# Kernel optimization log

Hardware: AMD Instinct MI355X
Metric: run time of the kernel (lower is better)

## Reference

```python
import jax, jax.numpy as jnp
import numpy as np
from jax.scipy.special import gammaln, logsumexp

T, K, D = 262144, 32, 64


def setup_inputs() -> dict:
    key = jax.random.key(0)
    ks = jax.random.split(key, 7)
    Y = jax.random.normal(ks[0], (T, D), dtype=jnp.float32)
    dT = jax.random.uniform(ks[1], (T,), dtype=jnp.float32) + 0.01  # strictly positive intervals
    A = jax.random.normal(ks[2], (K, K), dtype=jnp.float32)
    log_ab = jax.random.normal(ks[3], (K, 2), dtype=jnp.float32) * 0.5
    mu = jax.random.normal(ks[4], (K, D), dtype=jnp.float32)
    log_sigma = jax.random.normal(ks[5], (K, D), dtype=jnp.float32) * 0.1
    pi = jax.random.normal(ks[6], (K,), dtype=jnp.float32)
    return {"Y": Y, "dT": dT, "A": A, "log_ab": log_ab, "mu": mu, "log_sigma": log_sigma, "pi": pi}


def _gamma_ll(dT, log_ab):
    # per-state Gamma(concentration=exp(log_ab[:,0]), rate=exp(log_ab[:,1])) log_prob -> [T, K]
    a = jnp.exp(log_ab[:, 0])
    b = jnp.exp(log_ab[:, 1])
    const = a * log_ab[:, 1] - gammaln(a)  # a*log(b) - lgamma(a)
    return const[None, :] + jnp.log(dT)[:, None] * (a - 1.0)[None, :] - dT[:, None] * b[None, :]


def _gauss_ll(Y, mu, log_sigma):
    # diagonal-Gaussian emission log-likelihood summed over D, via GEMMs -> [T, K]
    inv_var = jnp.exp(-2.0 * log_sigma)  # [K, D]
    quad = (-0.5) * (Y * Y) @ inv_var.T + Y @ (mu * inv_var).T - 0.5 * jnp.sum(mu * mu * inv_var, axis=-1)[None, :]
    const = -jnp.sum(log_sigma, axis=-1) - 0.5 * D * jnp.log(2.0 * jnp.pi).astype(Y.dtype)
    return quad + const[None, :]


def _hmm_lognorm(pi0, logA, ll):
    # log-domain forward algorithm; returns log normalizer (scalar)
    alpha0 = pi0 + ll[0]

    def step(alpha, ll_t):
        # alpha_t[j] = logsumexp_i(alpha[i] + logA[i, j]) + ll_t[j]
        alpha = logsumexp(alpha[:, None] + logA, axis=0) + ll_t
        return alpha, None

    alphaT, _ = jax.lax.scan(step, alpha0, ll[1:])
    return logsumexp(alphaT)


def reference(Y, dT, A, log_ab, mu, log_sigma, pi):
    h = Y  # obs_model embedding (identity for Gaussian emission model)
    y_ll = _gauss_ll(Y, mu, log_sigma)          # [T, K]
    y_loss = jnp.zeros((), dtype=Y.dtype)
    dT_ll = _gamma_ll(dT, log_ab)               # [T, K]
    ll = y_ll + dT_ll
    logA = jax.nn.log_softmax(A, axis=1)        # LogSoftmax(dim=1)(A)
    pi0 = jax.nn.log_softmax(pi, axis=0)        # LogSoftmax(dim=0)(pi)
    loss = -1.0 * _hmm_lognorm(pi0, logA, ll) + y_loss
    return h, loss
```

## Files before the change

### kernel.cpp

```cpp
#include <hip/hip_runtime.h>
#include <stdint.h>

#define TT 262144
#define KK 32
#define DD 64
#define LSTEP 32
#define PCH 8192
#define YSTRIDE 68

typedef __attribute__((ext_vector_type(4)))  float f4v;
typedef __attribute__((ext_vector_type(16))) float f16v;
typedef __attribute__((ext_vector_type(4)))  short s4v;
typedef __attribute__((ext_vector_type(2)))  int   i2v;
typedef __attribute__((ext_vector_type(2)))  unsigned int u2v;
typedef __attribute__((ext_vector_type(4)))  unsigned int u4v;

#define WS_AFRAG_US 0
#define WS_WFRAG_US 1024
#define WS_WF    2560
#define WS_CK    6656
#define WS_AM1   6688
#define WS_BB    6720
#define WS_PI0   6752
#define WS_LS    8192
#define WS_LS2   16384
#define SH_MATS  33280
#define SH_MATS2 (33280 + PCH*1024)
#define LN2F 0.69314718055994531f

__device__ __forceinline__ unsigned pkbf(float hi, float lo) {
    return __builtin_amdgcn_perm(__builtin_bit_cast(unsigned, hi),
                                 __builtin_bit_cast(unsigned, lo), 0x07060302u);
}
__device__ __forceinline__ unsigned short f2bf_rne(float f) {
    unsigned u = __builtin_bit_cast(unsigned, f);
    unsigned r = u + 0x7FFFu + ((u >> 16) & 1u);
    return (unsigned short)(r >> 16);
}
__device__ __forceinline__ float bf2f(unsigned short u) {
    return __builtin_bit_cast(float, (unsigned)u << 16);
}
__device__ __forceinline__ float wmax32(float v) {
    v = fmaxf(v, __shfl_xor(v, 1));  v = fmaxf(v, __shfl_xor(v, 2));
    v = fmaxf(v, __shfl_xor(v, 4));  v = fmaxf(v, __shfl_xor(v, 8));
    v = fmaxf(v, __shfl_xor(v, 16));
    return v;
}
__device__ __forceinline__ float wmax64(float v) {
    v = wmax32(v); v = fmaxf(v, __shfl_xor(v, 32));
    return v;
}
__device__ __forceinline__ float wsum32(float v) {
    v += __shfl_xor(v, 1); v += __shfl_xor(v, 2); v += __shfl_xor(v, 4);
    v += __shfl_xor(v, 8); v += __shfl_xor(v, 16);
    return v;
}
__device__ __forceinline__ float wsum64(float v) {
    v = wsum32(v); v += __shfl_xor(v, 32);
    return v;
}
__device__ __forceinline__ float wval(int dd, int k, const float* mu, const float* lsg) {
    int d = dd & 63;
    float lv = lsg[k * DD + d];
    float iv = __expf(-2.f * lv);
    return (dd < DD) ? (-0.5f * iv) : (mu[k * DD + d] * iv);
}

__global__ void k0_prep(const float* __restrict__ Y, const float* __restrict__ A,
                        const float* __restrict__ lab, const float* __restrict__ mu,
                        const float* __restrict__ lsg, const float* __restrict__ pi,
                        float* __restrict__ ws, float* __restrict__ out)
{
    __shared__ float lseA[KK];
    const int tid = threadIdx.x;
    if (tid < KK) {
        float m = -1e30f;
        for (int j = 0; j < KK; ++j) m = fmaxf(m, A[tid * KK + j]);
        float s = 0.f;
        for (int j = 0; j < KK; ++j) s += __expf(A[tid * KK + j] - m);
        lseA[tid] = m + __logf(s);

        float mp = -1e30f;
        for (int j = 0; j < KK; ++j) mp = fmaxf(mp, pi[j]);
        float sp = 0.f;
        for (int j = 0; j < KK; ++j) sp += __expf(pi[j] - mp);
        ws[WS_PI0 + tid] = pi[tid] - (mp + __logf(sp));

        float la = lab[tid * 2 + 0], lb = lab[tid * 2 + 1];
        float a = __expf(la), b = __expf(lb);
        float c1 = 0.f, c2 = 0.f;
        for (int d = 0; d < DD; ++d) {
            float lv = lsg[tid * DD + d];
            float mv = mu[tid * DD + d];
            c1 -= lv;
            c2 += mv * mv * __expf(-2.f * lv);
        }
        ws[WS_CK + tid]  = a * lb - lgammaf(a) + c1 - 0.5f * c2 - 32.f * 1.8378770664093453f;
        ws[WS_AM1 + tid] = a - 1.f;
        ws[WS_BB + tid]  = b;
    }
    __syncthreads();
    unsigned short* us = (unsigned short*)ws;
    for (int idx = tid; idx < 1024; idx += 256) {
        int g = idx >> 8, rem = idx & 255, ln = rem >> 2, e = rem & 3;
        int m = 8 * g + 4 * (ln >> 5) + e, i = ln & 31;
        us[WS_AFRAG_US + idx] = f2bf_rne(__expf(A[m * KK + i] - lseA[m]));
    }
    for (int idx = tid; idx < 4096; idx += 256) {
        int s = idx >> 8, rem = idx & 255, ln = rem >> 2, e = rem & 3;
        int dd = 8 * s + 4 * (ln >> 5) + e, k = ln & 31;
        us[WS_WFRAG_US + idx] = f2bf_rne(wval(dd, k, mu, lsg));
    }
    for (int idx = tid; idx < 4096; idx += 256) {
        int dd = idx >> 5, k = idx & 31;
        ws[WS_WF + idx] = wval(dd, k, mu, lsg);
    }
    if (tid < DD) out[tid] = Y[tid];
}

__global__ __launch_bounds__(256, 4) void k1_scan(
    const float* __restrict__ Y, const float* __restrict__ dTp,
    float* __restrict__ ws, float* __restrict__ out)
{
    __shared__ __align__(16) float Yt[4][32 * YSTRIDE];
    __shared__ __align__(16) float dtv[4][32], dtl[4][32];

    const int tid = threadIdx.x;
    const int wv = tid >> 6, l = tid & 63, h = l >> 5, c = l & 31;
    const int p = blockIdx.x * 4 + wv;
    const int t0 = 1 + p * LSTEP;
    const int nsteps = min(LSTEP, TT - t0);

    const unsigned short* afr = (const unsigned short*)ws + WS_AFRAG_US;
    const unsigned short* wfr = (const unsigned short*)ws + WS_WFRAG_US;

    const float cK = ws[WS_CK + c], am1 = ws[WS_AM1 + c], bb = ws[WS_BB + c];

    if (l < 32) {
        int t = t0 + l;
        float dv = (t < TT) ? dTp[t] : 1.f;
        dtv[wv][l] = dv;
        dtl[wv][l] = __logf(dv);
    }

    f16v zf;
    #pragma unroll
    for (int r = 0; r < 16; ++r) zf[r] = 0.f;

    {
        const size_t gbase = (size_t)t0 * DD;
        const int r = (l >> 4);
        const int col = (l & 15) * 4;
        #pragma unroll
        for (int i = 0; i < 8; ++i) {
            const size_t gi = gbase + (size_t)i * 256 + l * 4;
            f4v y4; y4[0] = 0.f; y4[1] = 0.f; y4[2] = 0.f; y4[3] = 0.f;
            const bool ok = gi < (size_t)TT * DD;
            if (ok) y4 = *(const f4v*)(Y + gi);
            if (ok) *(f4v*)(out + gi) = y4;
            *(f4v*)(&Yt[wv][(i * 4 + r) * YSTRIDE + col]) = y4;
        }
    }

    f16v acc = zf;
    s4v rawf[8];
    #pragma unroll
    for (int g = 0; g < 8; ++g) {
        const f4v y4 = *(const f4v*)(&Yt[wv][c * YSTRIDE + 8 * g + 4 * h]);
        const f4v q4 = y4 * y4;
        i2v sq; sq[0] = pkbf(q4[1], q4[0]); sq[1] = pkbf(q4[3], q4[2]);
        i2v rw; rw[0] = pkbf(y4[1], y4[0]); rw[1] = pkbf(y4[3], y4[2]);
        rawf[g] = __builtin_bit_cast(s4v, rw);
        s4v wf = *(const s4v*)(wfr + g * 256 + l * 4);
        acc = __builtin_amdgcn_mfma_f32_32x32x8bf16_1k(__builtin_bit_cast(s4v, sq), wf, acc, 0, 0, 0);
    }
    #pragma unroll
    for (int g = 0; g < 8; ++g) {
        s4v wf = *(const s4v*)(wfr + (8 + g) * 256 + l * 4);
        acc = __builtin_amdgcn_mfma_f32_32x32x8bf16_1k(rawf[g], wf, acc, 0, 0, 0);
    }

    s4v aF[4];
    #pragma unroll
    for (int g = 0; g < 4; ++g) aF[g] = *(const s4v*)(afr + g * 256 + l * 4);

    float csv = 0.f;
    #pragma unroll
    for (int m = 0; m < 4; ++m) {
        const f4v dv4 = *(const f4v*)(&dtv[wv][8 * m + 4 * h]);
        const f4v dl4 = *(const f4v*)(&dtl[wv][8 * m + 4 * h]);
        #pragma unroll
        for (int j = 0; j < 4; ++j) {
            const int row = 8 * m + 4 * h + j;
            float llv = acc[4 * m + j] + cK + am1 * dl4[j] - bb * dv4[j];
            float cm = wmax32(llv);
            Yt[wv][row * YSTRIDE + c] = __expf(llv - cm);
            csv += (row < nsteps) ? cm : 0.f;
        }
    }
    float cacc = wsum64(csv) * (1.f / 32.f);

    asm volatile("s_waitcnt lgkmcnt(0)" ::: "memory");

    f16v S;
    #pragma unroll
    for (int m = 0; m < 4; ++m)
        #pragma unroll
        for (int j = 0; j < 4; ++j)
            S[4 * m + j] = ((8 * m + 4 * h + j) == c) ? 1.f : 0.f;
    float l2acc = 0.f;

    auto step = [&](int n) {
        f16v Dv = zf;
        #pragma unroll
        for (int g = 0; g < 4; ++g) {
            i2v bd; bd[0] = pkbf(S[4 * g + 1], S[4 * g + 0]);
                    bd[1] = pkbf(S[4 * g + 3], S[4 * g + 2]);
            Dv = __builtin_amdgcn_mfma_f32_32x32x8bf16_1k(aF[g], __builtin_bit_cast(s4v, bd), Dv, 0, 0, 0);
        }
        #pragma unroll
        for (int m = 0; m < 4; ++m) {
            const f4v e4 = *(const f4v*)(&Yt[wv][n * YSTRIDE + 8 * m + 4 * h]);
            #pragma unroll
            for (int j = 0; j < 4; ++j) S[4 * m + j] = Dv[4 * m + j] * e4[j];
        }
    };
    auto rescale = [&]() {
        float mx = S[0];
        #pragma unroll
        for (int r = 1; r < 16; ++r) mx = fmaxf(mx, S[r]);
        mx = wmax64(mx);
        const float inv = __fdividef(1.f, mx);
        #pragma unroll
        for (int r = 0; r < 16; ++r) S[r] *= inv;
        l2acc += __log2f(mx);
    };

    if (p != PCH - 1) {
        #pragma unroll
        for (int n = 0; n < LSTEP; ++n) {
            step(n);
            if ((n & 3) == 3) rescale();
        }
    } else {
        for (int n = 0; n < nsteps; ++n) {
            step(n);
            if ((n & 3) == 3) rescale();
        }
    }

    unsigned short* Tb = (unsigned short*)&Yt[wv][0];
    asm volatile("s_waitcnt lgkmcnt(0)" ::: "memory");
    #pragma unroll
    for (int m = 0; m < 4; ++m)
        #pragma unroll
        for (int j = 0; j < 4; ++j)
            Tb[(8 * m + 4 * h + j) * 36 + c] = f2bf_rne(S[4 * m + j]);
    asm volatile("s_waitcnt lgkmcnt(0)" ::: "memory");
    u2v tg[4];
    #pragma unroll
    for (int g = 0; g < 4; ++g)
        tg[g] = *(const u2v*)(Tb + c * 36 + 8 * g + 4 * h);
    unsigned short* gm = (unsigned short*)ws + SH_MATS + (size_t)p * 1024 + l * 16;
    u4v s0; s0[0] = tg[0][0]; s0[1] = tg[0][1]; s0[2] = tg[1][0]; s0[3] = tg[1][1];
    u4v s1; s1[0] = tg[2][0]; s1[1] = tg[2][1]; s1[2] = tg[3][0]; s1[3] = tg[3][1];
    *(u4v*)(gm) = s0;
    *(u4v*)(gm + 8) = s1;
    if (l == 0) ws[WS_LS + p] = cacc + LN2F * l2acc;
}

__device__ __forceinline__ f16v prodAU(const u4v a0, const u4v a1, const f16v U, const f16v zf) {
    s4v aA[4];
    u2v t;
    t[0] = a0[0]; t[1] = a0[1]; aA[0] = __builtin_bit_cast(s4v, t);
    t[0] = a0[2]; t[1] = a0[3]; aA[1] = __builtin_bit_cast(s4v, t);
    t[0] = a1[0]; t[1] = a1[1]; aA[2] = __builtin_bit_cast(s4v, t);
    t[0] = a1[2]; t[1] = a1[3]; aA[3] = __builtin_bit_cast(s4v, t);
    f16v Dv = zf;
    #pragma unroll
    for (int g = 0; g < 4; ++g) {
        i2v bd; bd[0] = pkbf(U[4 * g + 1], U[4 * g + 0]);
                bd[1] = pkbf(U[4 * g + 3], U[4 * g + 2]);
        Dv = __builtin_amdgcn_mfma_f32_32x32x8bf16_1k(aA[g], __builtin_bit_cast(s4v, bd), Dv, 0, 0, 0);
    }
    return Dv;
}

__global__ __launch_bounds__(128, 1) void k2_combine(float* __restrict__ ws)
{
    __shared__ __align__(16) unsigned short slot[2][1152];
    __shared__ float scl[2], lac[2];
    const int tid = threadIdx.x, wv = tid >> 6, l = tid & 63, h = l >> 5, c = l & 31;
    const int blk = blockIdx.x;
    const int idx0 = blk * 64 + wv * 32;
    const unsigned short* mats = (const unsigned short*)ws + SH_MATS;

    float lsv = (l < 32) ? ws[WS_LS + idx0 + l] : 0.f;
    float lssum = wsum64(lsv);

    f16v zf;
    #pragma unroll
    for (int r = 0; r < 16; ++r) zf[r] = 0.f;
    f16v U;
    #pragma unroll
    for (int m = 0; m < 4; ++m)
        #pragma unroll
        for (int j = 0; j < 4; ++j)
            U[4 * m + j] = ((8 * m + 4 * h + j) == c) ? 1.f : 0.f;
    float l2a = 0.f;

    u4v pf[2][2];
    {
        const u4v* mp0 = (const u4v*)(mats + (size_t)idx0 * 1024) + l * 2;
        const u4v* mp1 = (const u4v*)(mats + (size_t)(idx0 + 1) * 1024) + l * 2;
        pf[0][0] = mp0[0]; pf[0][1] = mp0[1];
        pf[1][0] = mp1[0]; pf[1][1] = mp1[1];
    }
    for (int q = 0; q < 32; ++q) {
        const u4v a0 = pf[q & 1][0], a1 = pf[q & 1][1];
        if (q + 2 < 32) {
            const u4v* mp = (const u4v*)(mats + (size_t)(idx0 + q + 2) * 1024) + l * 2;
            pf[q & 1][0] = mp[0]; pf[q & 1][1] = mp[1];
        }
        f16v Dv = prodAU(a0, a1, U, zf);
        if ((q & 3) == 3) {
            float mx = Dv[0];
            #pragma unroll
            for (int r = 1; r < 16; ++r) mx = fmaxf(mx, Dv[r]);
            mx = wmax64(mx);
            const float inv = __fdividef(1.f, mx);
            #pragma unroll
            for (int r = 0; r < 16; ++r) U[r] = Dv[r] * inv;
            l2a += __log2f(mx);
        } else {
            U = Dv;
        }
    }
    #pragma unroll
    for (int m = 0; m < 4; ++m)
        #pragma unroll
        for (int j = 0; j < 4; ++j)
            slot[wv][(8 * m + 4 * h + j) * 36 + c] = f2bf_rne(U[4 * m + j]);
    if (l == 0) { scl[wv] = lssum; lac[wv] = l2a; }
    __syncthreads();

    if (wv == 0) {
        u4v a0, a1;
        {
            u2v t0 = *(const u2v*)(&slot[1][c * 36 + 0 + 4 * h]);
            u2v t1 = *(const u2v*)(&slot[1][c * 36 + 8 + 4 * h]);
            u2v t2 = *(const u2v*)(&slot[1][c * 36 + 16 + 4 * h]);
            u2v t3 = *(const u2v*)(&slot[1][c * 36 + 24 + 4 * h]);
            a0[0] = t0[0]; a0[1] = t0[1]; a0[2] = t1[0]; a0[3] = t1[1];
            a1[0] = t2[0]; a1[1] = t2[1]; a1[2] = t3[0]; a1[3] = t3[1];
        }
        f16v Dv = prodAU(a0, a1, U, zf);
        float mx = Dv[0];
        #pragma unroll
        for (int r = 1; r < 16; ++r) mx = fmaxf(mx, Dv[r]);
        mx = wmax64(mx);
        const float inv = __fdividef(1.f, mx);
        #pragma unroll
        for (int r = 0; r < 16; ++r) U[r] = Dv[r] * inv;
        const float l2tot = lac[0] + lac[1] + __log2f(mx);
        asm volatile("s_waitcnt lgkmcnt(0)" ::: "memory");
        #pragma unroll
        for (int m = 0; m < 4; ++m)
            #pragma unroll
            for (int j = 0; j < 4; ++j)
                slot[0][(8 * m + 4 * h + j) * 36 + c] = f2bf_rne(U[4 * m + j]);
        asm volatile("s_waitcnt lgkmcnt(0)" ::: "memory");
        u2v tg[4];
        #pragma unroll
        for (int g = 0; g < 4; ++g)
            tg[g] = *(const u2v*)(&slot[0][c * 36 + 8 * g + 4 * h]);
        unsigned short* gm = (unsigned short*)ws + SH_MATS2 + (size_t)blk * 1024 + l * 16;
        u4v s0; s0[0] = tg[0][0]; s0[1] = tg[0][1]; s0[2] = tg[1][0]; s0[3] = tg[1][1];
        u4v s1; s1[0] = tg[2][0]; s1[1] = tg[2][1]; s1[2] = tg[3][0]; s1[3] = tg[3][1];
        *(u4v*)(gm) = s0;
        *(u4v*)(gm + 8) = s1;
        if (l == 0) ws[WS_LS2 + blk] = scl[0] + scl[1] + LN2F * l2tot;
    }
}

__global__ __launch_bounds__(1024, 1) void k3_final(
    const float* __restrict__ Y, const float* __restrict__ dTp,
    float* __restrict__ ws, float* __restrict__ out)
{
    __shared__ __align__(16) unsigned short slot[16][1152];
    __shared__ float sc[16];
    const int tid = threadIdx.x, wv = tid >> 6, l = tid & 63, h = l >> 5, c = l & 31;
    const unsigned short* mats2 = (const unsigned short*)ws + SH_MATS2;

    f16v zf;
    #pragma unroll
    for (int r = 0; r < 16; ++r) zf[r] = 0.f;

    const int idx0 = wv * 8;
    float lsv = (l < 8) ? ws[WS_LS2 + idx0 + l] : 0.f;
    float lssum = wsum64(lsv);
    f16v U;
    #pragma unroll
    for (int m = 0; m < 4; ++m)
        #pragma unroll
        for (int j = 0; j < 4; ++j)
            U[4 * m + j] = ((8 * m + 4 * h + j) == c) ? 1.f : 0.f;
    float l2a = 0.f;
    u4v pf[2][2];
    {
        const u4v* mp0 = (const u4v*)(mats2 + (size_t)idx0 * 1024) + l * 2;
        const u4v* mp1 = (const u4v*)(mats2 + (size_t)(idx0 + 1) * 1024) + l * 2;
        pf[0][0] = mp0[0]; pf[0][1] = mp0[1];
        pf[1][0] = mp1[0]; pf[1][1] = mp1[1];
    }
    for (int q = 0; q < 8; ++q) {
        const u4v a0 = pf[q & 1][0], a1 = pf[q & 1][1];
        if (q + 2 < 8) {
            const u4v* mp = (const u4v*)(mats2 + (size_t)(idx0 + q + 2) * 1024) + l * 2;
            pf[q & 1][0] = mp[0]; pf[q & 1][1] = mp[1];
        }
        f16v Dv = prodAU(a0, a1, U, zf);
        if ((q & 3) == 3) {
            float mx = Dv[0];
            #pragma unroll
            for (int r = 1; r < 16; ++r) mx = fmaxf(mx, Dv[r]);
            mx = wmax64(mx);
            const float inv = __fdividef(1.f, mx);
            #pragma unroll
            for (int r = 0; r < 16; ++r) U[r] = Dv[r] * inv;
            l2a += __log2f(mx);
        } else {
            U = Dv;
        }
    }
    #pragma unroll
    for (int m = 0; m < 4; ++m)
        #pragma unroll
        for (int j = 0; j < 4; ++j)
            slot[wv][(8 * m + 4 * h + j) * 36 + c] = f2bf_rne(U[4 * m + j]);
    if (l == 0) sc[wv] = lssum + LN2F * l2a;
    __syncthreads();

    for (int s = 1; s < 16; s <<= 1) {
        const int cnt = 16 / (2 * s);
        if (wv < cnt) {
            const int i = wv * 2 * s;
            s4v aA[4], bB[4];
            #pragma unroll
            for (int g = 0; g < 4; ++g) {
                u2v t = *(const u2v*)(&slot[i + s][c * 36 + 8 * g + 4 * h]);
                aA[g] = __builtin_bit_cast(s4v, t);
                s4v b;
                #pragma unroll
                for (int j = 0; j < 4; ++j)
                    b[j] = (short)slot[i][(8 * g + 4 * h + j) * 36 + c];
                bB[g] = b;
            }
            f16v Dv = zf;
            #pragma unroll
            for (int g = 0; g < 4; ++g)
                Dv = __builtin_amdgcn_mfma_f32_32x32x8bf16_1k(aA[g], bB[g], Dv, 0, 0, 0);
            float mx = Dv[0];
            #pragma unroll
            for (int r = 1; r < 16; ++r) mx = fmaxf(mx, Dv[r]);
            mx = wmax64(mx);
            const float inv = __fdividef(1.f, mx);
            #pragma unroll
            for (int m = 0; m < 4; ++m)
                #pragma unroll
                for (int j = 0; j < 4; ++j)
                    slot[i][(8 * m + 4 * h + j) * 36 + c] = f2bf_rne(Dv[4 * m + j] * inv);
            if (l == 0) sc[i] = sc[i] + sc[i + s] + __logf(mx);
        }
        __syncthreads();
    }

    if (wv == 0) {
        float acc = 0.f;
        const float* Wf = ws + WS_WF;
        for (int dd = 0; dd < 128; ++dd) {
            const float yv = Y[dd & 63];
            const float f = (dd < 64) ? yv * yv : yv;
            acc = fmaf(f, Wf[dd * 32 + c], acc);
        }
        const float dt0 = dTp[0];
        const float ll0 = acc + ws[WS_CK + c] + ws[WS_AM1 + c] * __logf(dt0) - ws[WS_BB + c] * dt0;
        const float av = ws[WS_PI0 + c] + ll0;
        const float c0 = wmax32(av);
        const float a0 = __expf(av - c0);
        float part = 0.f;
        #pragma unroll
        for (int i = 0; i < 16; ++i) {
            const int ii = 16 * h + i;
            const float m = bf2f(slot[0][c * 36 + ii]);
            const float ai = __shfl(a0, ii);
            part = fmaf(m, ai, part);
        }
        const float srow = part + __shfl_xor(part, 32);
        const float tot = wsum32(srow);
        if (l == 0) out[(size_t)TT * DD] = -(sc[0] + c0 + __logf(tot));
    }
}

extern "C" void kernel_launch(void* const* d_in, const int* in_sizes, int n_in,
                              void* d_out, int out_size, void* d_ws, size_t ws_size,
                              hipStream_t stream)
{
    const float* Y   = (const float*)d_in[0];
    const float* dTp = (const float*)d_in[1];
    const float* A   = (const float*)d_in[2];
    const float* lab = (const float*)d_in[3];
    const float* mu  = (const float*)d_in[4];
    const float* lsg = (const float*)d_in[5];
    const float* pi  = (const float*)d_in[6];
    float* out = (float*)d_out;
    float* ws  = (float*)d_ws;

    hipLaunchKernelGGL(k0_prep, dim3(1), dim3(256), 0, stream, Y, A, lab, mu, lsg, pi, ws, out);
    hipLaunchKernelGGL(k1_scan, dim3(PCH / 4), dim3(256), 0, stream, Y, dTp, ws, out);
    hipLaunchKernelGGL(k2_combine, dim3(128), dim3(128), 0, stream, ws);
    hipLaunchKernelGGL(k3_final, dim3(1), dim3(1024), 0, stream, Y, dTp, ws, out);
}
```

Baseline: 193.1 us.

## Use 32x32x16 bf16 MFMA and interleave two chunk scans per wave

Switches every MFMA from the 32x32x8 bf16 instruction to the gfx950 32x32x16 variant, halving instruction count and re-laying out the A and W fragments in the prep kernel to match. Each wave in the scan kernel now handles two independent chunks and alternates their serial step chains, so the latency of one dependent MFMA chain can overlap with the other. The emission MFMA now reads Y rows straight from global memory instead of staging them in LDS. In exchange, register pressure goes up, only half as many waves are launched, and Y is read twice (once for the copy to the output, once for the emission).

```diff
diff --git a/kernel.cpp b/kernel.cpp
--- a/kernel.cpp
+++ b/kernel.cpp
@@ -6,12 +6,12 @@
 #define DD 64
 #define LSTEP 32
 #define PCH 8192
-#define YSTRIDE 68
 
 typedef __attribute__((ext_vector_type(4)))  float f4v;
 typedef __attribute__((ext_vector_type(16))) float f16v;
 typedef __attribute__((ext_vector_type(4)))  short s4v;
-typedef __attribute__((ext_vector_type(2)))  int   i2v;
+typedef __attribute__((ext_vector_type(8)))  short s8v;
+typedef __attribute__((ext_vector_type(8)))  __bf16 bf8v;
 typedef __attribute__((ext_vector_type(2)))  unsigned int u2v;
 typedef __attribute__((ext_vector_type(4)))  unsigned int u4v;
 
@@ -64,6 +64,10 @@
     float lv = lsg[k * DD + d];
     float iv = __expf(-2.f * lv);
     return (dd < DD) ? (-0.5f * iv) : (mu[k * DD + d] * iv);
+}
+__device__ __forceinline__ f16v mfma16(s8v a, s8v b, f16v c) {
+    return __builtin_amdgcn_mfma_f32_32x32x16_bf16(
+        __builtin_bit_cast(bf8v, a), __builtin_bit_cast(bf8v, b), c, 0, 0, 0);
 }
 
 __global__ void k0_prep(const float* __restrict__ Y, const float* __restrict__ A,
@@ -102,14 +106,14 @@
     __syncthreads();
     unsigned short* us = (unsigned short*)ws;
     for (int idx = tid; idx < 1024; idx += 256) {
-        int g = idx >> 8, rem = idx & 255, ln = rem >> 2, e = rem & 3;
-        int m = 8 * g + 4 * (ln >> 5) + e, i = ln & 31;
+        int g2 = idx >> 9, rem = idx & 511, ln = rem >> 3, e = rem & 7;
+        int m = 16 * g2 + 8 * (e >> 2) + 4 * (ln >> 5) + (e & 3), i = ln & 31;
         us[WS_AFRAG_US + idx] = f2bf_rne(__expf(A[m * KK + i] - lseA[m]));
     }
     for (int idx = tid; idx < 4096; idx += 256) {
-        int s = idx >> 8, rem = idx & 255, ln = rem >> 2, e = rem & 3;
-        int dd = 8 * s + 4 * (ln >> 5) + e, k = ln & 31;
-        us[WS_WFRAG_US + idx] = f2bf_rne(wval(dd, k, mu, lsg));
+        int s2 = idx >> 9, rem = idx & 511, ln = rem >> 3, e = rem & 7;
+        int dd = 16 * s2 + 8 * (e >> 2) + 4 * (ln >> 5) + (e & 3);
+        us[WS_WFRAG_US + idx] = f2bf_rne(wval(dd, ln & 31, mu, lsg));
     }
     for (int idx = tid; idx < 4096; idx += 256) {
         int dd = idx >> 5, k = idx & 31;
@@ -122,22 +126,23 @@
     const float* __restrict__ Y, const float* __restrict__ dTp,
     float* __restrict__ ws, float* __restrict__ out)
 {
-    __shared__ __align__(16) float Yt[4][32 * YSTRIDE];
-    __shared__ __align__(16) float dtv[4][32], dtl[4][32];
+    __shared__ __align__(16) float Ebuf[4][2][1152];
+    __shared__ __align__(16) float dtv[4][64], dtl[4][64];
 
     const int tid = threadIdx.x;
     const int wv = tid >> 6, l = tid & 63, h = l >> 5, c = l & 31;
-    const int p = blockIdx.x * 4 + wv;
-    const int t0 = 1 + p * LSTEP;
-    const int nsteps = min(LSTEP, TT - t0);
+    const int pA = (blockIdx.x * 4 + wv) * 2;
+    const int pB = pA + 1;
+    const int t0A = 1 + pA * LSTEP;
+    const int t0B = t0A + LSTEP;
 
     const unsigned short* afr = (const unsigned short*)ws + WS_AFRAG_US;
     const unsigned short* wfr = (const unsigned short*)ws + WS_WFRAG_US;
 
     const float cK = ws[WS_CK + c], am1 = ws[WS_AM1 + c], bb = ws[WS_BB + c];
 
-    if (l < 32) {
-        int t = t0 + l;
+    {
+        int t = t0A + l;
         float dv = (t < TT) ? dTp[t] : 1.f;
         dtv[wv][l] = dv;
         dtl[wv][l] = __logf(dv);
@@ -148,84 +153,111 @@
     for (int r = 0; r < 16; ++r) zf[r] = 0.f;
 
     {
-        const size_t gbase = (size_t)t0 * DD;
-        const int r = (l >> 4);
-        const int col = (l & 15) * 4;
-        #pragma unroll
-        for (int i = 0; i < 8; ++i) {
+        const size_t gbase = (size_t)t0A * DD;
+        #pragma unroll
+        for (int i = 0; i < 16; ++i) {
             const size_t gi = gbase + (size_t)i * 256 + l * 4;
-            f4v y4; y4[0] = 0.f; y4[1] = 0.f; y4[2] = 0.f; y4[3] = 0.f;
-            const bool ok = gi < (size_t)TT * DD;
-            if (ok) y4 = *(const f4v*)(Y + gi);
-            if (ok) *(f4v*)(out + gi) = y4;
-            *(f4v*)(&Yt[wv][(i * 4 + r) * YSTRIDE + col]) = y4;
-        }
-    }
-
-    f16v acc = zf;
-    s4v rawf[8];
-    #pragma unroll
-    for (int g = 0; g < 8; ++g) {
-        const f4v y4 = *(const f4v*)(&Yt[wv][c * YSTRIDE + 8 * g + 4 * h]);
-        const f4v q4 = y4 * y4;
-        i2v sq; sq[0] = pkbf(q4[1], q4[0]); sq[1] = pkbf(q4[3], q4[2]);
-        i2v rw; rw[0] = pkbf(y4[1], y4[0]); rw[1] = pkbf(y4[3], y4[2]);
-        rawf[g] = __builtin_bit_cast(s4v, rw);
-        s4v wf = *(const s4v*)(wfr + g * 256 + l * 4);
-        acc = __builtin_amdgcn_mfma_f32_32x32x8bf16_1k(__builtin_bit_cast(s4v, sq), wf, acc, 0, 0, 0);
-    }
-    #pragma unroll
-    for (int g = 0; g < 8; ++g) {
-        s4v wf = *(const s4v*)(wfr + (8 + g) * 256 + l * 4);
-        acc = __builtin_amdgcn_mfma_f32_32x32x8bf16_1k(rawf[g], wf, acc, 0, 0, 0);
-    }
-
-    s4v aF[4];
-    #pragma unroll
-    for (int g = 0; g < 4; ++g) aF[g] = *(const s4v*)(afr + g * 256 + l * 4);
-
-    float csv = 0.f;
-    #pragma unroll
-    for (int m = 0; m < 4; ++m) {
-        const f4v dv4 = *(const f4v*)(&dtv[wv][8 * m + 4 * h]);
-        const f4v dl4 = *(const f4v*)(&dtl[wv][8 * m + 4 * h]);
+            if (gi < (size_t)TT * DD) {
+                f4v y4 = *(const f4v*)(Y + gi);
+                *(f4v*)(out + gi) = y4;
+            }
+        }
+    }
+
+    s8v wfv[8];
+    #pragma unroll
+    for (int s2 = 0; s2 < 8; ++s2) wfv[s2] = *(const s8v*)(wfr + s2 * 512 + l * 8);
+
+    auto emit = [&](int t0) -> f16v {
+        f16v acc = zf;
+        s8v raws[4];
+        const bool ok = (t0 + c) < TT;
+        const float* yrow = Y + (size_t)(t0 + c) * DD;
+        #pragma unroll
+        for (int g2 = 0; g2 < 4; ++g2) {
+            f4v y0, y1;
+            y0[0]=0.f; y0[1]=0.f; y0[2]=0.f; y0[3]=0.f;
+            y1[0]=0.f; y1[1]=0.f; y1[2]=0.f; y1[3]=0.f;
+            if (ok) {
+                y0 = *(const f4v*)(yrow + 16 * g2 + 4 * h);
+                y1 = *(const f4v*)(yrow + 16 * g2 + 8 + 4 * h);
+            }
+            const f4v q0 = y0 * y0, q1 = y1 * y1;
+            u4v sqp, rwp;
+            sqp[0] = pkbf(q0[1], q0[0]); sqp[1] = pkbf(q0[3], q0[2]);
+            sqp[2] = pkbf(q1[1], q1[0]); sqp[3] = pkbf(q1[3], q1[2]);
+            rwp[0] = pkbf(y0[1], y0[0]); rwp[1] = pkbf(y0[3], y0[2]);
+            rwp[2] = pkbf(y1[1], y1[0]); rwp[3] = pkbf(y1[3], y1[2]);
+            raws[g2] = __builtin_bit_cast(s8v, rwp);
+            acc = mfma16(__builtin_bit_cast(s8v, sqp), wfv[g2], acc);
+        }
+        #pragma unroll
+        for (int g2 = 0; g2 < 4; ++g2)
+            acc = mfma16(raws[g2], wfv[4 + g2], acc);
+        return acc;
+    };
+
+    const f16v accA = emit(t0A);
+    const f16v accB = emit(t0B);
+
+    const s8v aF0 = *(const s8v*)(afr + l * 8);
+    const s8v aF1 = *(const s8v*)(afr + 512 + l * 8);
+
+    auto llphase = [&](const f16v& acc, int ch, int nsteps) -> float {
+        float csv = 0.f;
+        float* E = &Ebuf[wv][ch][0];
+        #pragma unroll
+        for (int m = 0; m < 4; ++m) {
+            const f4v dv4 = *(const f4v*)(&dtv[wv][ch * 32 + 8 * m + 4 * h]);
+            const f4v dl4 = *(const f4v*)(&dtl[wv][ch * 32 + 8 * m + 4 * h]);
+            #pragma unroll
+            for (int j = 0; j < 4; ++j) {
+                const int row = 8 * m + 4 * h + j;
+                float llv = acc[4 * m + j] + cK + am1 * dl4[j] - bb * dv4[j];
+                float cm = wmax32(llv);
+                E[row * 36 + c] = __expf(llv - cm);
+                csv += (row < nsteps) ? cm : 0.f;
+            }
+        }
+        return wsum64(csv) * (1.f / 32.f);
+    };
+    const int nsB = (pB == PCH - 1) ? (TT - t0B) : LSTEP;
+    const float caccA = llphase(accA, 0, LSTEP);
+    const float caccB = llphase(accB, 1, nsB);
+
+    asm volatile("s_waitcnt lgkmcnt(0)" ::: "memory");
+
+    f16v SA, SB;
+    #pragma unroll
+    for (int m = 0; m < 4; ++m)
         #pragma unroll
         for (int j = 0; j < 4; ++j) {
-            const int row = 8 * m + 4 * h + j;
-            float llv = acc[4 * m + j] + cK + am1 * dl4[j] - bb * dv4[j];
-            float cm = wmax32(llv);
-            Yt[wv][row * YSTRIDE + c] = __expf(llv - cm);
-            csv += (row < nsteps) ? cm : 0.f;
-        }
-    }
-    float cacc = wsum64(csv) * (1.f / 32.f);
-
-    asm volatile("s_waitcnt lgkmcnt(0)" ::: "memory");
-
-    f16v S;
-    #pragma unroll
-    for (int m = 0; m < 4; ++m)
-        #pragma unroll
-        for (int j = 0; j < 4; ++j)
-            S[4 * m + j] = ((8 * m + 4 * h + j) == c) ? 1.f : 0.f;
-    float l2acc = 0.f;
-
-    auto step = [&](int n) {
-        f16v Dv = zf;
-        #pragma unroll
-        for (int g = 0; g < 4; ++g) {
-            i2v bd; bd[0] = pkbf(S[4 * g + 1], S[4 * g + 0]);
-                    bd[1] = pkbf(S[4 * g + 3], S[4 * g + 2]);
-            Dv = __builtin_amdgcn_mfma_f32_32x32x8bf16_1k(aF[g], __builtin_bit_cast(s4v, bd), Dv, 0, 0, 0);
-        }
+            const float id = ((8 * m + 4 * h + j) == c) ? 1.f : 0.f;
+            SA[4 * m + j] = id;
+            SB[4 * m + j] = id;
+        }
+    float l2A = 0.f, l2B = 0.f;
+    const float* EA = &Ebuf[wv][0][0];
+    const float* EB = &Ebuf[wv][1][0];
+
+    auto step = [&](f16v& S, const float* E, int n) {
+        u4v b0, b1;
+        b0[0] = pkbf(S[1],  S[0]);  b0[1] = pkbf(S[3],  S[2]);
+        b0[2] = pkbf(S[5],  S[4]);  b0[3] = pkbf(S[7],  S[6]);
+        b1[0] = pkbf(S[9],  S[8]);  b1[1] = pkbf(S[11], S[10]);
+        b1[2] = pkbf(S[13], S[12]); b1[3] = pkbf(S[15], S[14]);
+        f16v Dv = mfma16(aF0, __builtin_bit_cast(s8v, b0), zf);
+        Dv = mfma16(aF1, __builtin_bit_cast(s8v, b1), Dv);
         #pragma unroll
         for (int m = 0; m < 4; ++m) {
-            const f4v e4 = *(const f4v*)(&Yt[wv][n * YSTRIDE + 8 * m + 4 * h]);
-            #pragma unroll
-            for (int j = 0; j < 4; ++j) S[4 * m + j] = Dv[4 * m + j] * e4[j];
+            const f4v e4 = *(const f4v*)(E + n * 36 + 8 * m + 4 * h);
+            S[4 * m + 0] = Dv[4 * m + 0] * e4[0];
+            S[4 * m + 1] = Dv[4 * m + 1] * e4[1];
+            S[4 * m + 2] = Dv[4 * m + 2] * e4[2];
+            S[4 * m + 3] = Dv[4 * m + 3] * e4[3];
         }
     };
-    auto rescale = [&]() {
+    auto rescale = [&](f16v& S, float& l2) {
         float mx = S[0];
         #pragma unroll
         for (int r = 1; r < 16; ++r) mx = fmaxf(mx, S[r]);
@@ -233,56 +265,56 @@
         const float inv = __fdividef(1.f, mx);
         #pragma unroll
         for (int r = 0; r < 16; ++r) S[r] *= inv;
-        l2acc += __log2f(mx);
+        l2 += __log2f(mx);
     };
 
-    if (p != PCH - 1) {
+    if (pB != PCH - 1) {
         #pragma unroll
         for (int n = 0; n < LSTEP; ++n) {
-            step(n);
-            if ((n & 3) == 3) rescale();
+            step(SA, EA, n);
+            step(SB, EB, n);
+            if ((n & 3) == 3) { rescale(SA, l2A); rescale(SB, l2B); }
         }
     } else {
-        for (int n = 0; n < nsteps; ++n) {
-            step(n);
-            if ((n & 3) == 3) rescale();
-        }
-    }
-
-    unsigned short* Tb = (unsigned short*)&Yt[wv][0];
-    asm volatile("s_waitcnt lgkmcnt(0)" ::: "memory");
-    #pragma unroll
-    for (int m = 0; m < 4; ++m)
-        #pragma unroll
-        for (int j = 0; j < 4; ++j)
-            Tb[(8 * m + 4 * h + j) * 36 + c] = f2bf_rne(S[4 * m + j]);
-    asm volatile("s_waitcnt lgkmcnt(0)" ::: "memory");
-    u2v tg[4];
-    #pragma unroll
-    for (int g = 0; g < 4; ++g)
-        tg[g] = *(const u2v*)(Tb + c * 36 + 8 * g + 4 * h);
-    unsigned short* gm = (unsigned short*)ws + SH_MATS + (size_t)p * 1024 + l * 16;
-    u4v s0; s0[0] = tg[0][0]; s0[1] = tg[0][1]; s0[2] = tg[1][0]; s0[3] = tg[1][1];
-    u4v s1; s1[0] = tg[2][0]; s1[1] = tg[2][1]; s1[2] = tg[3][0]; s1[3] = tg[3][1];
-    *(u4v*)(gm) = s0;
-    *(u4v*)(gm + 8) = s1;
-    if (l == 0) ws[WS_LS + p] = cacc + LN2F * l2acc;
+        for (int n = 0; n < LSTEP; ++n) {
+            step(SA, EA, n);
+            if (n < nsB) step(SB, EB, n);
+            if ((n & 3) == 3) { rescale(SA, l2A); rescale(SB, l2B); }
+        }
+    }
+
+    auto storemat = [&](const f16v& S, int ch, int p, float cacc, float l2) {
+        unsigned short* Tb = (unsigned short*)&Ebuf[wv][ch][0];
+        asm volatile("s_waitcnt lgkmcnt(0)" ::: "memory");
+        #pragma unroll
+        for (int m = 0; m < 4; ++m)
+            #pragma unroll
+            for (int j = 0; j < 4; ++j)
+                Tb[(8 * m + 4 * h + j) * 36 + c] = f2bf_rne(S[4 * m + j]);
+        asm volatile("s_waitcnt lgkmcnt(0)" ::: "memory");
+        u2v tg0 = *(const u2v*)(Tb + c * 36 + 0  + 4 * h);
+        u2v tg1 = *(const u2v*)(Tb + c * 36 + 8  + 4 * h);
+        u2v tg2 = *(const u2v*)(Tb + c * 36 + 16 + 4 * h);
+        u2v tg3 = *(const u2v*)(Tb + c * 36 + 24 + 4 * h);
+        unsigned short* gm = (unsigned short*)ws + SH_MATS + (size_t)p * 1024 + l * 16;
+        u4v s0; s0[0] = tg0[0]; s0[1] = tg0[1]; s0[2] = tg1[0]; s0[3] = tg1[1];
+        u4v s1; s1[0] = tg2[0]; s1[1] = tg2[1]; s1[2] = tg3[0]; s1[3] = tg3[1];
+        *(u4v*)(gm) = s0;
+        *(u4v*)(gm + 8) = s1;
+        if (l == 0) ws[WS_LS + p] = cacc + LN2F * l2;
+    };
+    storemat(SA, 0, pA, caccA, l2A);
+    storemat(SB, 1, pB, caccB, l2B);
 }
 
 __device__ __forceinline__ f16v prodAU(const u4v a0, const u4v a1, const f16v U, const f16v zf) {
-    s4v aA[4];
-    u2v t;
-    t[0] = a0[0]; t[1] = a0[1]; aA[0] = __builtin_bit_cast(s4v, t);
-    t[0] = a0[2]; t[1] = a0[3]; aA[1] = __builtin_bit_cast(s4v, t);
-    t[0] = a1[0]; t[1] = a1[1]; aA[2] = __builtin_bit_cast(s4v, t);
-    t[0] = a1[2]; t[1] = a1[3]; aA[3] = __builtin_bit_cast(s4v, t);
-    f16v Dv = zf;
-    #pragma unroll
-    for (int g = 0; g < 4; ++g) {
-        i2v bd; bd[0] = pkbf(U[4 * g + 1], U[4 * g + 0]);
-                bd[1] = pkbf(U[4 * g + 3], U[4 * g + 2]);
-        Dv = __builtin_amdgcn_mfma_f32_32x32x8bf16_1k(aA[g], __builtin_bit_cast(s4v, bd), Dv, 0, 0, 0);
-    }
+    u4v b0, b1;
+    b0[0] = pkbf(U[1],  U[0]);  b0[1] = pkbf(U[3],  U[2]);
+    b0[2] = pkbf(U[5],  U[4]);  b0[3] = pkbf(U[7],  U[6]);
+    b1[0] = pkbf(U[9],  U[8]);  b1[1] = pkbf(U[11], U[10]);
+    b1[2] = pkbf(U[13], U[12]); b1[3] = pkbf(U[15], U[14]);
+    f16v Dv = mfma16(__builtin_bit_cast(s8v, a0), __builtin_bit_cast(s8v, b0), zf);
+    Dv = mfma16(__builtin_bit_cast(s8v, a1), __builtin_bit_cast(s8v, b1), Dv);
     return Dv;
 }
 
@@ -445,21 +477,26 @@
         const int cnt = 16 / (2 * s);
         if (wv < cnt) {
             const int i = wv * 2 * s;
-            s4v aA[4], bB[4];
-            #pragma unroll
-            for (int g = 0; g < 4; ++g) {
-                u2v t = *(const u2v*)(&slot[i + s][c * 36 + 8 * g + 4 * h]);
-                aA[g] = __builtin_bit_cast(s4v, t);
-                s4v b;
+            s8v aA0, aA1, bB0, bB1;
+            {
+                u2v t0 = *(const u2v*)(&slot[i + s][c * 36 + 0 + 4 * h]);
+                u2v t1 = *(const u2v*)(&slot[i + s][c * 36 + 8 + 4 * h]);
+                u2v t2 = *(const u2v*)(&slot[i + s][c * 36 + 16 + 4 * h]);
+                u2v t3 = *(const u2v*)(&slot[i + s][c * 36 + 24 + 4 * h]);
+                u4v a0; a0[0] = t0[0]; a0[1] = t0[1]; a0[2] = t1[0]; a0[3] = t1[1];
+                u4v a1; a1[0] = t2[0]; a1[1] = t2[1]; a1[2] = t3[0]; a1[3] = t3[1];
+                aA0 = __builtin_bit_cast(s8v, a0);
+                aA1 = __builtin_bit_cast(s8v, a1);
                 #pragma unroll
-                for (int j = 0; j < 4; ++j)
-                    b[j] = (short)slot[i][(8 * g + 4 * h + j) * 36 + c];
-                bB[g] = b;
+                for (int j = 0; j < 4; ++j) {
+                    bB0[j]     = (short)slot[i][(0  + 4 * h + j) * 36 + c];
+                    bB0[4 + j] = (short)slot[i][(8  + 4 * h + j) * 36 + c];
+                    bB1[j]     = (short)slot[i][(16 + 4 * h + j) * 36 + c];
+                    bB1[4 + j] = (short)slot[i][(24 + 4 * h + j) * 36 + c];
+                }
             }
-            f16v Dv = zf;
-            #pragma unroll
-            for (int g = 0; g < 4; ++g)
-                Dv = __builtin_amdgcn_mfma_f32_32x32x8bf16_1k(aA[g], bB[g], Dv, 0, 0, 0);
+            f16v Dv = mfma16(aA0, bB0, zf);
+            Dv = mfma16(aA1, bB1, Dv);
             float mx = Dv[0];
             #pragma unroll
             for (int r = 1; r < 16; ++r) mx = fmaxf(mx, Dv[r]);
@@ -517,7 +554,7 @@
     float* ws  = (float*)d_ws;
 
     hipLaunchKernelGGL(k0_prep, dim3(1), dim3(256), 0, stream, Y, A, lab, mu, lsg, pi, ws, out);
-    hipLaunchKernelGGL(k1_scan, dim3(PCH / 4), dim3(256), 0, stream, Y, dTp, ws, out);
+    hipLaunchKernelGGL(k1_scan, dim3(PCH / 8), dim3(256), 0, stream, Y, dTp, ws, out);
     hipLaunchKernelGGL(k2_combine, dim3(128), dim3(128), 0, stream, ws);
     hipLaunchKernelGGL(k3_final, dim3(1), dim3(1024), 0, stream, Y, dTp, ws, out);
 }
```

After: 199.0 us. 3.1% more time.
